# Kernel tuning notes

Measured on AMD Instinct MI355X. Metric: run time of the kernel, lower is better.

## Reference

```python
import jax, jax.numpy as jnp
import numpy as np

B, T, IN, H, OUT = 128, 1024, 17, 512, 17


def setup_inputs() -> dict:
    key = jax.random.key(0)
    ks = jax.random.split(key, 11)
    s_in = 1.0 / np.sqrt(H)
    return {
        "x": jax.random.normal(ks[0], (B, T, IN), dtype=jnp.float32),
        "wih0": jax.random.normal(ks[1], (4 * H, IN), dtype=jnp.float32) * s_in,
        "whh0": jax.random.normal(ks[2], (4 * H, H), dtype=jnp.float32) * s_in,
        "bih0": jax.random.normal(ks[3], (4 * H,), dtype=jnp.float32) * s_in,
        "bhh0": jax.random.normal(ks[4], (4 * H,), dtype=jnp.float32) * s_in,
        "wih1": jax.random.normal(ks[5], (4 * H, H), dtype=jnp.float32) * s_in,
        "whh1": jax.random.normal(ks[6], (4 * H, H), dtype=jnp.float32) * s_in,
        "bih1": jax.random.normal(ks[7], (4 * H,), dtype=jnp.float32) * s_in,
        "bhh1": jax.random.normal(ks[8], (4 * H,), dtype=jnp.float32) * s_in,
        "lin_w": jax.random.normal(ks[9], (OUT, H), dtype=jnp.float32) * s_in,
        "lin_b": jax.random.normal(ks[10], (OUT,), dtype=jnp.float32) * s_in,
    }


def _lstm_layer(x, wih, whh, bih, bhh):
    # x: [B, T, D]; gate order i, f, g, o (torch.nn.LSTMCell convention)
    b, _, _ = x.shape
    h = whh.shape[1]
    # Precompute input projection for all timesteps: [B, T, 4H]
    proj = jnp.einsum("btd,gd->btg", x, wih) + bih

    def step(carry, p_t):
        h_t, c_t = carry
        gates = p_t + h_t @ whh.T + bhh  # [B, 4H]
        i, f, g, o = jnp.split(gates, 4, axis=1)
        i = jax.nn.sigmoid(i)
        f = jax.nn.sigmoid(f)
        o = jax.nn.sigmoid(o)
        g = jnp.tanh(g)
        c_t = f * c_t + i * g
        h_t = o * jnp.tanh(c_t)
        return (h_t, c_t), h_t

    h0 = jnp.zeros((b, h), x.dtype)
    c0 = jnp.zeros((b, h), x.dtype)
    _, ys = jax.lax.scan(step, (h0, c0), jnp.swapaxes(proj, 0, 1))  # ys: [T, B, H]
    return jnp.swapaxes(ys, 0, 1)  # [B, T, H]


def reference(x, wih0, whh0, bih0, bhh0, wih1, whh1, bih1, bhh1, lin_w, lin_b):
    y = _lstm_layer(x, wih0, whh0, bih0, bhh0)
    y = _lstm_layer(y, wih1, whh1, bih1, bhh1)
    h_last = y[:, -1, :]  # [B, H]
    return h_last @ lin_w.T + lin_b  # [B, OUT]
```

## Files before the change

kernel.cpp:

```cpp
#include <hip/hip_runtime.h>
#include <cstddef>
#include <cstdint>

typedef unsigned long long ull;
typedef unsigned short u16;
typedef __attribute__((ext_vector_type(8))) short s8v;
typedef __attribute__((ext_vector_type(4))) float f4v;

#define GROUPS 8
#define BG     16
#define JS     16
#define TPB    256
#define NT     1024
#define HDIM   512
#define INDIM  17
#define OUTDIM 17
#define BTOT   128

#define AT_LD(p)   __hip_atomic_load((p), __ATOMIC_RELAXED, __HIP_MEMORY_SCOPE_AGENT)
#define AT_ST(p,v) __hip_atomic_store((p), (v), __ATOMIC_RELAXED, __HIP_MEMORY_SCOPE_AGENT)

#define TILE_U16 8192
#define WIDX(k, b) ((((k) >> 5) * 512) + ((((k) >> 3) & 3) * 128) + ((b) * 8) + ((k) & 7))

#define FA_OFF     ((size_t)0)
#define FB_OFF     ((size_t)16384)
#define RA_OFF     ((size_t)32768)
#define RING_BYTES ((size_t)4 * GROUPS * 2 * TILE_U16 * 2)
#define RB_OFF     (RA_OFF + RING_BYTES)
#define WS_NEEDED  (RB_OFF + RING_BYTES)
#define RIX(sl, gr, pl) ((((size_t)(sl) * GROUPS + (gr)) * 2 + (pl)) * TILE_U16)

#define L_H0   0
#define L_H1   98304
#define L_EXA  131072
#define L_EXB  135168
#define L_CTL  139264
#define LDS_SZ 139328

__device__ __forceinline__ u16 f2bf(float f) {
  unsigned int u = __float_as_uint(f);
  u += 0x7FFFu + ((u >> 16) & 1u);
  return (u16)(u >> 16);
}
__device__ __forceinline__ float bf2f(u16 h) {
  return __uint_as_float(((unsigned int)h) << 16);
}
__device__ __forceinline__ float sigm(float x) { return 1.f / (1.f + __expf(-x)); }
__device__ __forceinline__ float tanh_f(float x) { return 2.f / (1.f + __expf(-2.f * x)) - 1.f; }

#define MFMA(a, b, c) __builtin_amdgcn_mfma_f32_16x16x32_bf16((a), (b), (c), 0, 0, 0)

__device__ __forceinline__ void pbar(int* c, int& nbar, int lane) {
  ++nbar;
  if (lane == 0)
    (void)__hip_atomic_fetch_add(c, 1, __ATOMIC_RELEASE, __HIP_MEMORY_SCOPE_WORKGROUP);
  while (__hip_atomic_load(c, __ATOMIC_ACQUIRE, __HIP_MEMORY_SCOPE_WORKGROUP) < 2 * nbar) {}
}

__global__ __launch_bounds__(TPB, 1) void lstm_fused(
    const float* __restrict__ x,
    const float* __restrict__ wih0, const float* __restrict__ whh0,
    const float* __restrict__ bih0, const float* __restrict__ bhh0,
    const float* __restrict__ wih1, const float* __restrict__ whh1,
    const float* __restrict__ bih1, const float* __restrict__ bhh1,
    u16* __restrict__ ringA, u16* __restrict__ ringB,
    int* __restrict__ flagsA, int* __restrict__ flagsB)
{
  const int bid  = blockIdx.x;
  const int gr   = bid & 7;
  const int wg   = bid >> 3;
  const int j0   = wg * JS;
  const int tid  = threadIdx.x;
  const int wave = tid >> 6;
  const int lane = tid & 63;
  const int n    = lane & 15;
  const int q    = lane >> 4;
  const int k0   = q * 8;

  __shared__ __align__(16) char smem[LDS_SZ];
  int* ctl = (int*)(smem + L_CTL);
  float* exgA = (float*)(smem + L_EXA);
  float* exgB = (float*)(smem + L_EXB);

  if (tid < 8) ctl[tid] = 0;

  {
    int b_l = tid >> 4, j_l = tid & 15, jg = j0 + j_l;
    int wo = WIDX(jg, b_l);
    AT_ST(&ringA[RIX(0, gr, 0) + wo], (u16)0);
    AT_ST(&ringA[RIX(0, gr, 1) + wo], (u16)0);
    AT_ST(&ringB[RIX(0, gr, 0) + wo], (u16)0);
    AT_ST(&ringB[RIX(0, gr, 1) + wo], (u16)0);
  }
  __syncthreads();
  if (wave == 0 && lane == 0) AT_ST(flagsA + bid * 16, 1);
  if (wave == 2 && lane == 0) AT_ST(flagsB + bid * 16, 1);

  const f4v z = {0.f, 0.f, 0.f, 0.f};
  const int p  = (wave & 1) * 64 + lane;
  const int jq = p & 15, b0 = p >> 4;
  const int jg = j0 + jq;
  const int wo0 = WIDX(jg, b0), wo1 = WIDX(jg, b0 + 8);

  if (wave < 2) {
    const int g0 = wave * 2;
    s8v wx_h[2], wx_l[2];
#pragma unroll
    for (int i = 0; i < 2; ++i) {
      const float* wr = wih0 + (size_t)((g0 + i) * HDIM + j0 + n) * INDIM;
#pragma unroll
      for (int j = 0; j < 8; ++j) {
        int k = k0 + j;
        float v = (k < INDIM) ? wr[k] : 0.f;
        u16 hi = f2bf(v);
        wx_h[i][j] = (short)hi;
        wx_l[i][j] = (short)f2bf(v - bf2f(hi));
      }
    }
    s8v wh_h[2][16], wh_l[2][16];
#pragma unroll
    for (int i = 0; i < 2; ++i) {
      const float* wr = whh0 + (size_t)((g0 + i) * HDIM + j0 + n) * HDIM;
#pragma unroll
      for (int kt = 0; kt < 16; ++kt)
#pragma unroll
        for (int j = 0; j < 8; ++j) {
          float v = wr[kt * 32 + k0 + j];
          u16 hi = f2bf(v);
          wh_h[i][kt][j] = (short)hi;
          wh_l[i][kt][j] = (short)f2bf(v - bf2f(hi));
        }
    }
    float bias[4];
#pragma unroll
    for (int g = 0; g < 4; ++g) bias[g] = bih0[g * HDIM + jg] + bhh0[g * HDIM + jg];
    float c0a = 0.f, c0b = 0.f;
    int nbar = 0;

    for (int s = 1; s <= NT + 1; ++s) {
      f4v xa[2] = {z, z};
      if (s <= NT) {
        const float* xr = x + ((size_t)(gr * BG + n) * NT + (s - 1)) * INDIM;
        s8v axh, axl;
#pragma unroll
        for (int j = 0; j < 8; ++j) {
          int k = k0 + j;
          float v = (k < INDIM) ? xr[k] : 0.f;
          u16 hi = f2bf(v);
          axh[j] = (short)hi;
          axl[j] = (short)f2bf(v - bf2f(hi));
        }
#pragma unroll
        for (int i = 0; i < 2; ++i) {
          xa[i] = MFMA(axh, wx_h[i], xa[i]);
          xa[i] = MFMA(axl, wx_h[i], xa[i]);
          xa[i] = MFMA(axh, wx_l[i], xa[i]);
        }
      }
      if (wave == 0) {
        const int* pp = (lane < 32) ? (flagsA + (lane * 8 + gr) * 16)
                                    : (flagsB + ((lane & 31) * 8 + gr) * 16);
        const int tgt = (lane < 32) ? s : s - 3;
        while (__ballot(AT_LD(pp) >= tgt) != ~0ULL) __builtin_amdgcn_s_sleep(1);
        __hip_atomic_store(&ctl[2], s, __ATOMIC_RELEASE, __HIP_MEMORY_SCOPE_WORKGROUP);
      } else {
        while (__hip_atomic_load(&ctl[2], __ATOMIC_ACQUIRE, __HIP_MEMORY_SCOPE_WORKGROUP) < s) {}
      }
      const int sl3 = (s - 1) % 3;
      {
        const ull* src = (const ull*)(ringA + RIX((s - 1) & 3, gr, wave));
        char* dst = smem + L_H0 + (sl3 * 2 + wave) * 16384;
#pragma unroll
        for (int r = 0; r < 32; r += 16) {
          ull v[16];
#pragma unroll
          for (int i = 0; i < 16; ++i) v[i] = AT_LD(src + (r + i) * 64 + lane);
#pragma unroll
          for (int i = 0; i < 16; ++i) *(ull*)(dst + ((r + i) * 64 + lane) * 8) = v[i];
        }
      }
      pbar(&ctl[0], nbar, lane);
      if (wave == 0 && lane == 0)
        __hip_atomic_store(&ctl[4 + sl3], s - 1, __ATOMIC_RELEASE,
                           __HIP_MEMORY_SCOPE_WORKGROUP);
      if (s == NT + 1) break;

      const char* sh = smem + L_H0 + (sl3 * 2 + 0) * 16384;
      const char* sl = smem + L_H0 + (sl3 * 2 + 1) * 16384;
      f4v cHH[2] = {z, z}, cLH[2] = {z, z}, cHL[2] = {z, z};
#pragma unroll
      for (int kt = 0; kt < 16; ++kt) {
        s8v ah = *(const s8v*)(sh + kt * 1024 + q * 256 + n * 16);
        s8v al = *(const s8v*)(sl + kt * 1024 + q * 256 + n * 16);
#pragma unroll
        for (int i = 0; i < 2; ++i) {
          cHH[i] = MFMA(ah, wh_h[i][kt], cHH[i]);
          cLH[i] = MFMA(al, wh_h[i][kt], cLH[i]);
          cHL[i] = MFMA(ah, wh_l[i][kt], cHL[i]);
        }
      }
#pragma unroll
      for (int i = 0; i < 2; ++i) {
        f4v e = xa[i] + cHH[i] + cLH[i] + cHL[i];
#pragma unroll
        for (int r = 0; r < 4; ++r)
          exgA[(g0 + i) * 256 + (q * 4 + r) * 16 + n] = e[r];
      }
      pbar(&ctl[0], nbar, lane);
      float pr0[4], pr1[4];
#pragma unroll
      for (int g = 0; g < 4; ++g) {
        pr0[g] = exgA[g * 256 + b0 * 16 + jq] + bias[g];
        pr1[g] = exgA[g * 256 + (b0 + 8) * 16 + jq] + bias[g];
      }
      {
        float ig = sigm(pr0[0]), fg = sigm(pr0[1]), gg = tanh_f(pr0[2]), og = sigm(pr0[3]);
        c0a = fg * c0a + ig * gg;
        float h = og * tanh_f(c0a);
        u16 hh = f2bf(h), hl = f2bf(h - bf2f(hh));
        AT_ST(&ringA[RIX(s & 3, gr, 0) + wo0], hh);
        AT_ST(&ringA[RIX(s & 3, gr, 1) + wo0], hl);
      }
      {
        float ig = sigm(pr1[0]), fg = sigm(pr1[1]), gg = tanh_f(pr1[2]), og = sigm(pr1[3]);
        c0b = fg * c0b + ig * gg;
        float h = og * tanh_f(c0b);
        u16 hh = f2bf(h), hl = f2bf(h - bf2f(hh));
        AT_ST(&ringA[RIX(s & 3, gr, 0) + wo1], hh);
        AT_ST(&ringA[RIX(s & 3, gr, 1) + wo1], hl);
      }
      __asm__ volatile("s_waitcnt vmcnt(0)" ::: "memory");
      pbar(&ctl[0], nbar, lane);
      if (wave == 0 && lane == 0) AT_ST(flagsA + bid * 16, s + 1);
    }
  } else {
    const int wv = wave - 2;
    const int g0 = wv * 2;
    s8v w1x[2][16], w1h[2][16];
#pragma unroll
    for (int i = 0; i < 2; ++i) {
      const float* p1 = wih1 + (size_t)((g0 + i) * HDIM + j0 + n) * HDIM;
      const float* p2 = whh1 + (size_t)((g0 + i) * HDIM + j0 + n) * HDIM;
#pragma unroll
      for (int kt = 0; kt < 16; ++kt)
#pragma unroll
        for (int j = 0; j < 8; ++j) {
          w1x[i][kt][j] = (short)f2bf(p1[kt * 32 + k0 + j]);
          w1h[i][kt][j] = (short)f2bf(p2[kt * 32 + k0 + j]);
        }
    }
    float bias[4];
#pragma unroll
    for (int g = 0; g < 4; ++g) bias[g] = bih1[g * HDIM + jg] + bhh1[g * HDIM + jg];
    float c1a = 0.f, c1b = 0.f;
    int nbar = 0;

    for (int t = 1; t <= NT; ++t) {
      if (wave == 2) {
        const int* pp = flagsB + ((lane & 31) * 8 + gr) * 16;
        while (__ballot(AT_LD(pp) >= t) != ~0ULL) __builtin_amdgcn_s_sleep(1);
        __hip_atomic_store(&ctl[3], t, __ATOMIC_RELEASE, __HIP_MEMORY_SCOPE_WORKGROUP);
      } else {
        while (__hip_atomic_load(&ctl[3], __ATOMIC_ACQUIRE, __HIP_MEMORY_SCOPE_WORKGROUP) < t) {}
      }
      {
        const ull* src = (const ull*)(ringB + RIX((t - 1) & 3, gr, wv));
        char* dst = smem + L_H1 + wv * 16384;
#pragma unroll
        for (int r = 0; r < 32; r += 16) {
          ull v[16];
#pragma unroll
          for (int i = 0; i < 16; ++i) v[i] = AT_LD(src + (r + i) * 64 + lane);
#pragma unroll
          for (int i = 0; i < 16; ++i) *(ull*)(dst + ((r + i) * 64 + lane) * 8) = v[i];
        }
      }
      pbar(&ctl[1], nbar, lane);
      const char* th = smem + L_H1;
      const char* tl = smem + L_H1 + 16384;
      f4v dHH[2] = {z, z}, dLH[2] = {z, z};
#pragma unroll
      for (int kt = 0; kt < 16; ++kt) {
        s8v ah = *(const s8v*)(th + kt * 1024 + q * 256 + n * 16);
        s8v al = *(const s8v*)(tl + kt * 1024 + q * 256 + n * 16);
#pragma unroll
        for (int i = 0; i < 2; ++i) {
          dHH[i] = MFMA(ah, w1h[i][kt], dHH[i]);
          dLH[i] = MFMA(al, w1h[i][kt], dLH[i]);
        }
      }
      const int sl3 = t % 3;
      while (__hip_atomic_load(&ctl[4 + sl3], __ATOMIC_ACQUIRE,
                               __HIP_MEMORY_SCOPE_WORKGROUP) < t) {}
      const char* sh = smem + L_H0 + (sl3 * 2 + 0) * 16384;
      const char* sl = smem + L_H0 + (sl3 * 2 + 1) * 16384;
      f4v eHH[2] = {z, z}, eLH[2] = {z, z};
#pragma unroll
      for (int kt = 0; kt < 16; ++kt) {
        s8v ah = *(const s8v*)(sh + kt * 1024 + q * 256 + n * 16);
        s8v al = *(const s8v*)(sl + kt * 1024 + q * 256 + n * 16);
#pragma unroll
        for (int i = 0; i < 2; ++i) {
          eHH[i] = MFMA(ah, w1x[i][kt], eHH[i]);
          eLH[i] = MFMA(al, w1x[i][kt], eLH[i]);
        }
      }
#pragma unroll
      for (int i = 0; i < 2; ++i) {
        f4v e = dHH[i] + dLH[i] + eHH[i] + eLH[i];
#pragma unroll
        for (int r = 0; r < 4; ++r)
          exgB[(g0 + i) * 256 + (q * 4 + r) * 16 + n] = e[r];
      }
      pbar(&ctl[1], nbar, lane);
      float pr0[4], pr1[4];
#pragma unroll
      for (int g = 0; g < 4; ++g) {
        pr0[g] = exgB[g * 256 + b0 * 16 + jq] + bias[g];
        pr1[g] = exgB[g * 256 + (b0 + 8) * 16 + jq] + bias[g];
      }
      {
        float ig = sigm(pr0[0]), fg = sigm(pr0[1]), gg = tanh_f(pr0[2]), og = sigm(pr0[3]);
        c1a = fg * c1a + ig * gg;
        float h = og * tanh_f(c1a);
        u16 hh = f2bf(h), hl = f2bf(h - bf2f(hh));
        AT_ST(&ringB[RIX(t & 3, gr, 0) + wo0], hh);
        AT_ST(&ringB[RIX(t & 3, gr, 1) + wo0], hl);
      }
      {
        float ig = sigm(pr1[0]), fg = sigm(pr1[1]), gg = tanh_f(pr1[2]), og = sigm(pr1[3]);
        c1b = fg * c1b + ig * gg;
        float h = og * tanh_f(c1b);
        u16 hh = f2bf(h), hl = f2bf(h - bf2f(hh));
        AT_ST(&ringB[RIX(t & 3, gr, 0) + wo1], hh);
        AT_ST(&ringB[RIX(t & 3, gr, 1) + wo1], hl);
      }
      __asm__ volatile("s_waitcnt vmcnt(0)" ::: "memory");
      pbar(&ctl[1], nbar, lane);
      if (wave == 2 && lane == 0) AT_ST(flagsB + bid * 16, t + 1);
    }
  }
}

__global__ void final_linear(const u16* __restrict__ ringB,
                             const float* __restrict__ lin_w,
                             const float* __restrict__ lin_b,
                             float* __restrict__ out) {
  int b = blockIdx.x, o = threadIdx.x;
  int gr = b >> 4, b_l = b & 15;
  if (o < OUTDIM) {
    float acc = lin_b[o];
    const u16* ph = ringB + RIX(NT & 3, gr, 0);
    const u16* pl = ringB + RIX(NT & 3, gr, 1);
    for (int j = 0; j < HDIM; ++j) {
      int idx = WIDX(j, b_l);
      float h = bf2f(ph[idx]) + bf2f(pl[idx]);
      acc += h * lin_w[(size_t)o * HDIM + j];
    }
    out[b * OUTDIM + o] = acc;
  }
}

__global__ void init_flags(int* __restrict__ f) {
  int i = blockIdx.x * TPB + threadIdx.x;
  if (i < 2 * 4096) f[i] = 0;
}

__global__ void sentinel_kernel(float* __restrict__ out, int nv) {
  int i = blockIdx.x * TPB + threadIdx.x;
  if (i < nv) out[i] = 1e30f;
}

extern "C" void kernel_launch(void* const* d_in, const int* in_sizes, int n_in,
                              void* d_out, int out_size, void* d_ws, size_t ws_size,
                              hipStream_t stream) {
  (void)in_sizes; (void)n_in;
  const float* x     = (const float*)d_in[0];
  const float* wih0  = (const float*)d_in[1];
  const float* whh0  = (const float*)d_in[2];
  const float* bih0  = (const float*)d_in[3];
  const float* bhh0  = (const float*)d_in[4];
  const float* wih1  = (const float*)d_in[5];
  const float* whh1  = (const float*)d_in[6];
  const float* bih1  = (const float*)d_in[7];
  const float* bhh1  = (const float*)d_in[8];
  const float* lin_w = (const float*)d_in[9];
  const float* lin_b = (const float*)d_in[10];
  float* out = (float*)d_out;
  char* ws = (char*)d_ws;

  if (ws_size < WS_NEEDED) {
    sentinel_kernel<<<(out_size + TPB - 1) / TPB, TPB, 0, stream>>>(out, out_size);
    return;
  }

  int* flagsA = (int*)(ws + FA_OFF);
  int* flagsB = (int*)(ws + FB_OFF);
  u16* ringA  = (u16*)(ws + RA_OFF);
  u16* ringB  = (u16*)(ws + RB_OFF);

  init_flags<<<(2 * 4096 + TPB - 1) / TPB, TPB, 0, stream>>>(flagsA);
  lstm_fused<<<256, TPB, 0, stream>>>(x, wih0, whh0, bih0, bhh0,
                                      wih1, whh1, bih1, bhh1,
                                      ringA, ringB, flagsA, flagsB);
  final_linear<<<BTOT, 64, 0, stream>>>(ringB, lin_w, lin_b, out);
}
```

Baseline: 4.993 ms.

## Stage hidden-state outputs in LDS and publish with one coalesced wave store

Each LSTM cell now writes its bf16 hi/lo hidden outputs into a small LDS staging buffer. After the barrier, a single wave copies the workgroup's contiguous slice to the global ring with 64-bit stores, waits, and sets the flag. This replaces scattered 16-bit atomic stores from all waves and the full-block vmcnt wait. The per-workgroup progress flags are also packed contiguously per group instead of padded on separate 64-byte lines. Packing the flags shrinks the polling footprint but may add cache-line contention between writers.

```diff
diff --git a/kernel.cpp b/kernel.cpp
--- a/kernel.cpp
+++ b/kernel.cpp
@@ -22,10 +22,11 @@
 
 #define TILE_U16 8192
 #define WIDX(k, b) ((((k) >> 5) * 512) + ((((k) >> 3) & 3) * 128) + ((b) * 8) + ((k) & 7))
+#define SLICE(wg)  (((wg) >> 1) * 512 + ((wg) & 1) * 256)
 
 #define FA_OFF     ((size_t)0)
-#define FB_OFF     ((size_t)16384)
-#define RA_OFF     ((size_t)32768)
+#define FB_OFF     ((size_t)1024)
+#define RA_OFF     ((size_t)4096)
 #define RING_BYTES ((size_t)4 * GROUPS * 2 * TILE_U16 * 2)
 #define RB_OFF     (RA_OFF + RING_BYTES)
 #define WS_NEEDED  (RB_OFF + RING_BYTES)
@@ -35,8 +36,10 @@
 #define L_H1   98304
 #define L_EXA  131072
 #define L_EXB  135168
-#define L_CTL  139264
-#define LDS_SZ 139328
+#define L_HOA  139264
+#define L_HOB  140288
+#define L_CTL  141312
+#define LDS_SZ 141376
 
 __device__ __forceinline__ u16 f2bf(float f) {
   unsigned int u = __float_as_uint(f);
@@ -94,14 +97,16 @@
     AT_ST(&ringB[RIX(0, gr, 1) + wo], (u16)0);
   }
   __syncthreads();
-  if (wave == 0 && lane == 0) AT_ST(flagsA + bid * 16, 1);
-  if (wave == 2 && lane == 0) AT_ST(flagsB + bid * 16, 1);
+  if (wave == 0 && lane == 0) AT_ST(flagsA + gr * 32 + wg, 1);
+  if (wave == 2 && lane == 0) AT_ST(flagsB + gr * 32 + wg, 1);
 
   const f4v z = {0.f, 0.f, 0.f, 0.f};
   const int p  = (wave & 1) * 64 + lane;
   const int jq = p & 15, b0 = p >> 4;
   const int jg = j0 + jq;
-  const int wo0 = WIDX(jg, b0), wo1 = WIDX(jg, b0 + 8);
+  const int ho0 = (jq >> 3) * 128 + b0 * 8 + (jq & 7);
+  const int ho1 = (jq >> 3) * 128 + (b0 + 8) * 8 + (jq & 7);
+  const int slice = SLICE(wg);
 
   if (wave < 2) {
     const int g0 = wave * 2;
@@ -159,8 +164,9 @@
         }
       }
       if (wave == 0) {
-        const int* pp = (lane < 32) ? (flagsA + (lane * 8 + gr) * 16)
-                                    : (flagsB + ((lane & 31) * 8 + gr) * 16);
+        const int idx = lane & 31;
+        const int* pp = (lane < 32) ? (flagsA + gr * 32 + idx)
+                                    : (flagsB + gr * 32 + idx);
         const int tgt = (lane < 32) ? s : s - 3;
         while (__ballot(AT_LD(pp) >= tgt) != ~0ULL) __builtin_amdgcn_s_sleep(1);
         __hip_atomic_store(&ctl[2], s, __ATOMIC_RELEASE, __HIP_MEMORY_SCOPE_WORKGROUP);
@@ -208,31 +214,41 @@
           exgA[(g0 + i) * 256 + (q * 4 + r) * 16 + n] = e[r];
       }
       pbar(&ctl[0], nbar, lane);
-      float pr0[4], pr1[4];
-#pragma unroll
-      for (int g = 0; g < 4; ++g) {
-        pr0[g] = exgA[g * 256 + b0 * 16 + jq] + bias[g];
-        pr1[g] = exgA[g * 256 + (b0 + 8) * 16 + jq] + bias[g];
-      }
-      {
-        float ig = sigm(pr0[0]), fg = sigm(pr0[1]), gg = tanh_f(pr0[2]), og = sigm(pr0[3]);
+      u16* hoh = (u16*)(smem + L_HOA);
+      u16* hol = (u16*)(smem + L_HOA + 512);
+      {
+        float pi = exgA[0 * 256 + b0 * 16 + jq] + bias[0];
+        float pf = exgA[1 * 256 + b0 * 16 + jq] + bias[1];
+        float pg = exgA[2 * 256 + b0 * 16 + jq] + bias[2];
+        float po = exgA[3 * 256 + b0 * 16 + jq] + bias[3];
+        float ig = sigm(pi), fg = sigm(pf), gg = tanh_f(pg), og = sigm(po);
         c0a = fg * c0a + ig * gg;
         float h = og * tanh_f(c0a);
         u16 hh = f2bf(h), hl = f2bf(h - bf2f(hh));
-        AT_ST(&ringA[RIX(s & 3, gr, 0) + wo0], hh);
-        AT_ST(&ringA[RIX(s & 3, gr, 1) + wo0], hl);
-      }
-      {
-        float ig = sigm(pr1[0]), fg = sigm(pr1[1]), gg = tanh_f(pr1[2]), og = sigm(pr1[3]);
+        hoh[ho0] = hh; hol[ho0] = hl;
+      }
+      {
+        float pi = exgA[0 * 256 + (b0 + 8) * 16 + jq] + bias[0];
+        float pf = exgA[1 * 256 + (b0 + 8) * 16 + jq] + bias[1];
+        float pg = exgA[2 * 256 + (b0 + 8) * 16 + jq] + bias[2];
+        float po = exgA[3 * 256 + (b0 + 8) * 16 + jq] + bias[3];
+        float ig = sigm(pi), fg = sigm(pf), gg = tanh_f(pg), og = sigm(po);
         c0b = fg * c0b + ig * gg;
         float h = og * tanh_f(c0b);
         u16 hh = f2bf(h), hl = f2bf(h - bf2f(hh));
-        AT_ST(&ringA[RIX(s & 3, gr, 0) + wo1], hh);
-        AT_ST(&ringA[RIX(s & 3, gr, 1) + wo1], hl);
-      }
-      __asm__ volatile("s_waitcnt vmcnt(0)" ::: "memory");
+        hoh[ho1] = hh; hol[ho1] = hl;
+      }
       pbar(&ctl[0], nbar, lane);
-      if (wave == 0 && lane == 0) AT_ST(flagsA + bid * 16, s + 1);
+      if (wave == 0) {
+        ull v0 = *(const ull*)(smem + L_HOA + lane * 8);
+        ull v1 = *(const ull*)(smem + L_HOA + 512 + lane * 8);
+        ull* d0 = (ull*)ringA + ((RIX(s & 3, gr, 0) + slice) >> 2);
+        ull* d1 = (ull*)ringA + ((RIX(s & 3, gr, 1) + slice) >> 2);
+        AT_ST(d0 + lane, v0);
+        AT_ST(d1 + lane, v1);
+        __asm__ volatile("s_waitcnt vmcnt(0)" ::: "memory");
+        if (lane == 0) AT_ST(flagsA + gr * 32 + wg, s + 1);
+      }
     }
   } else {
     const int wv = wave - 2;
@@ -258,7 +274,7 @@
 
     for (int t = 1; t <= NT; ++t) {
       if (wave == 2) {
-        const int* pp = flagsB + ((lane & 31) * 8 + gr) * 16;
+        const int* pp = flagsB + gr * 32 + (lane & 31);
         while (__ballot(AT_LD(pp) >= t) != ~0ULL) __builtin_amdgcn_s_sleep(1);
         __hip_atomic_store(&ctl[3], t, __ATOMIC_RELEASE, __HIP_MEMORY_SCOPE_WORKGROUP);
       } else {
@@ -314,31 +330,41 @@
           exgB[(g0 + i) * 256 + (q * 4 + r) * 16 + n] = e[r];
       }
       pbar(&ctl[1], nbar, lane);
-      float pr0[4], pr1[4];
-#pragma unroll
-      for (int g = 0; g < 4; ++g) {
-        pr0[g] = exgB[g * 256 + b0 * 16 + jq] + bias[g];
-        pr1[g] = exgB[g * 256 + (b0 + 8) * 16 + jq] + bias[g];
-      }
-      {
-        float ig = sigm(pr0[0]), fg = sigm(pr0[1]), gg = tanh_f(pr0[2]), og = sigm(pr0[3]);
+      u16* hoh = (u16*)(smem + L_HOB);
+      u16* hol = (u16*)(smem + L_HOB + 512);
+      {
+        float pi = exgB[0 * 256 + b0 * 16 + jq] + bias[0];
+        float pf = exgB[1 * 256 + b0 * 16 + jq] + bias[1];
+        float pg = exgB[2 * 256 + b0 * 16 + jq] + bias[2];
+        float po = exgB[3 * 256 + b0 * 16 + jq] + bias[3];
+        float ig = sigm(pi), fg = sigm(pf), gg = tanh_f(pg), og = sigm(po);
         c1a = fg * c1a + ig * gg;
         float h = og * tanh_f(c1a);
         u16 hh = f2bf(h), hl = f2bf(h - bf2f(hh));
-        AT_ST(&ringB[RIX(t & 3, gr, 0) + wo0], hh);
-        AT_ST(&ringB[RIX(t & 3, gr, 1) + wo0], hl);
-      }
-      {
-        float ig = sigm(pr1[0]), fg = sigm(pr1[1]), gg = tanh_f(pr1[2]), og = sigm(pr1[3]);
+        hoh[ho0] = hh; hol[ho0] = hl;
+      }
+      {
+        float pi = exgB[0 * 256 + (b0 + 8) * 16 + jq] + bias[0];
+        float pf = exgB[1 * 256 + (b0 + 8) * 16 + jq] + bias[1];
+        float pg = exgB[2 * 256 + (b0 + 8) * 16 + jq] + bias[2];
+        float po = exgB[3 * 256 + (b0 + 8) * 16 + jq] + bias[3];
+        float ig = sigm(pi), fg = sigm(pf), gg = tanh_f(pg), og = sigm(po);
         c1b = fg * c1b + ig * gg;
         float h = og * tanh_f(c1b);
         u16 hh = f2bf(h), hl = f2bf(h - bf2f(hh));
-        AT_ST(&ringB[RIX(t & 3, gr, 0) + wo1], hh);
-        AT_ST(&ringB[RIX(t & 3, gr, 1) + wo1], hl);
-      }
-      __asm__ volatile("s_waitcnt vmcnt(0)" ::: "memory");
+        hoh[ho1] = hh; hol[ho1] = hl;
+      }
       pbar(&ctl[1], nbar, lane);
-      if (wave == 2 && lane == 0) AT_ST(flagsB + bid * 16, t + 1);
+      if (wave == 2) {
+        ull v0 = *(const ull*)(smem + L_HOB + lane * 8);
+        ull v1 = *(const ull*)(smem + L_HOB + 512 + lane * 8);
+        ull* d0 = (ull*)ringB + ((RIX(t & 3, gr, 0) + slice) >> 2);
+        ull* d1 = (ull*)ringB + ((RIX(t & 3, gr, 1) + slice) >> 2);
+        AT_ST(d0 + lane, v0);
+        AT_ST(d1 + lane, v1);
+        __asm__ volatile("s_waitcnt vmcnt(0)" ::: "memory");
+        if (lane == 0) AT_ST(flagsB + gr * 32 + wg, t + 1);
+      }
     }
   }
 }
@@ -364,7 +390,7 @@
 
 __global__ void init_flags(int* __restrict__ f) {
   int i = blockIdx.x * TPB + threadIdx.x;
-  if (i < 2 * 4096) f[i] = 0;
+  if (i < 512) f[i] = 0;
 }
 
 __global__ void sentinel_kernel(float* __restrict__ out, int nv) {
@@ -400,7 +426,7 @@
   u16* ringA  = (u16*)(ws + RA_OFF);
   u16* ringB  = (u16*)(ws + RB_OFF);
 
-  init_flags<<<(2 * 4096 + TPB - 1) / TPB, TPB, 0, stream>>>(flagsA);
+  init_flags<<<2, TPB, 0, stream>>>(flagsA);
   lstm_fused<<<256, TPB, 0, stream>>>(x, wih0, whh0, bih0, bhh0,
                                       wih1, whh1, bih1, bhh1,
                                       ringA, ringB, flagsA, flagsB);
```

After: 5.274 ms. 1.06x slower.
